# Optimization experiments

Hardware: AMD Instinct MI355X
Metric: run time of the kernel (lower is better)

Reference implementation:

```python
import jax, jax.numpy as jnp
import numpy as np

L, N, E = 2048, 2, 1024
H = 16                      # num_heads
DH = E // H                 # head_dim = 64
SCALE = DH ** -0.5
NEG = -10000.0


def setup_inputs() -> dict:
    key = jax.random.key(0)
    ks = jax.random.split(key, 9)
    s = 0.02
    return {
        "query": jax.random.normal(ks[0], (L, N, E), jnp.float32),
        "q_proj": jax.random.normal(ks[1], (E, E), jnp.float32) * s,
        "q_bias": jax.random.normal(ks[2], (E,), jnp.float32) * s,
        "k_proj": jax.random.normal(ks[3], (E, E), jnp.float32) * s,
        "k_bias": jax.random.normal(ks[4], (E,), jnp.float32) * s,
        "v_proj": jax.random.normal(ks[5], (E, E), jnp.float32) * s,
        "v_bias": jax.random.normal(ks[6], (E,), jnp.float32) * s,
        "out_proj": jax.random.normal(ks[7], (E, E), jnp.float32) * s,
        "out_bias": jax.random.normal(ks[8], (E,), jnp.float32) * s,
    }


def reference(query, q_proj, q_bias, k_proj, k_bias, v_proj, v_bias, out_proj, out_bias):
    # query: [L, N, E]; projections act as F.linear: x @ W.T + b
    q = query @ q_proj.T + q_bias
    k = query @ k_proj.T + k_bias
    v = query @ v_proj.T + v_bias
    # [L, N*H, DH] -> [N*H, L, DH]
    q = q.reshape(L, N * H, DH).transpose(1, 0, 2) * SCALE
    k = k.reshape(L, N * H, DH).transpose(1, 0, 2)
    v = v.reshape(L, N * H, DH).transpose(1, 0, 2)
    attn = jnp.einsum('bqd,bkd->bqk', q, k)  # [N*H, L, L]
    causal = jnp.tril(jnp.ones((L, L), jnp.float32)) < 0.5  # True above diagonal
    attn = jnp.where(causal[None, :, :], NEG, attn)
    attn = jax.nn.softmax(attn, axis=-1)
    # dropout_p = 0.0 in training mode -> identity
    out = jnp.einsum('bqk,bkd->bqd', attn, v)  # [N*H, L, DH]
    out = out.transpose(1, 0, 2).reshape(L, N, H * DH)
    return out @ out_proj.T + out_bias
```

## Files before the change

kernel.cpp:

```cpp
#include <hip/hip_runtime.h>
#include <stdint.h>

typedef __attribute__((ext_vector_type(8)))  short          bf16x8;
typedef __attribute__((ext_vector_type(4)))  float          f32x4;
typedef __attribute__((ext_vector_type(16))) float          f32x16;
typedef __attribute__((ext_vector_type(4)))  unsigned int   u32x4;
typedef __attribute__((ext_vector_type(4)))  unsigned short u16x4;

#define SCALE_LOG2E 0.180336880f

static __device__ __forceinline__ unsigned short f2bf(float x) {
  union { float f; unsigned int u; } c; c.f = x;
  unsigned int r = c.u + 0x7fffu + ((c.u >> 16) & 1u);
  return (unsigned short)(r >> 16);
}

static __device__ __forceinline__ unsigned int cvt_pk_bf16(float lo, float hi) {
  unsigned int r;
  asm volatile("v_cvt_pk_bf16_f32 %0, %1, %2" : "=v"(r) : "v"(lo), "v"(hi));
  return r;
}

static __device__ __forceinline__ void stage16(const unsigned short* g, unsigned short* l) {
  __builtin_amdgcn_global_load_lds(
      (const __attribute__((address_space(1))) unsigned int*)g,
      (__attribute__((address_space(3)))       unsigned int*)l, 16, 0, 0);
}

__global__ __launch_bounds__(256) void cvt_f32_bf16(const float* __restrict__ src,
                                                    unsigned short* __restrict__ dst, int n) {
  int i = (blockIdx.x * 256 + threadIdx.x) * 4;
  if (i < n) {
    float4 v = *(const float4*)(src + i);
    u16x4 o; o.x = f2bf(v.x); o.y = f2bf(v.y); o.z = f2bf(v.z); o.w = f2bf(v.w);
    *(u16x4*)(dst + i) = o;
  }
}

__global__ __launch_bounds__(256) void cvt_w4(const float* __restrict__ wq, const float* __restrict__ wk,
                                              const float* __restrict__ wv, const float* __restrict__ wo,
                                              unsigned short* __restrict__ dst) {
  const int z = blockIdx.y;
  const float* src = z == 0 ? wq : (z == 1 ? wk : (z == 2 ? wv : wo));
  int i = (blockIdx.x * 256 + threadIdx.x) * 4;
  float4 v = *(const float4*)(src + i);
  u16x4 o; o.x = f2bf(v.x); o.y = f2bf(v.y); o.z = f2bf(v.z); o.w = f2bf(v.w);
  *(u16x4*)(dst + (size_t)z * 1048576 + i) = o;
}

__device__ __forceinline__ void gemm_tile_core(const unsigned short* __restrict__ A,
                                               const unsigned short* __restrict__ B,
                                               int bi, int bj, f32x4 (&acc)[4][4]) {
  __shared__ unsigned short As[128 * 32];
  __shared__ unsigned short Bs[128 * 32];
  const int t = threadIdx.x, w = t >> 6, l = t & 63;
  const int l15 = l & 15, l4 = l >> 4;
  const int wm = w >> 1, wn = w & 1;
  const int srow = l >> 2, scol = (l & 3) * 8;

#pragma unroll
  for (int m = 0; m < 4; m++)
#pragma unroll
    for (int n = 0; n < 4; n++)
#pragma unroll
      for (int r = 0; r < 4; r++) acc[m][n][r] = 0.f;

  const int koff = 8 * l4;
  for (int k0 = 0; k0 < 1024; k0 += 32) {
    stage16(A + (size_t)(bi * 128 + w * 16 + srow) * 1024 + k0 + scol, (unsigned short*)As + w * 512);
    stage16(A + (size_t)(bi * 128 + (w + 4) * 16 + srow) * 1024 + k0 + scol, (unsigned short*)As + (w + 4) * 512);
    stage16(B + (size_t)(bj * 128 + w * 16 + srow) * 1024 + k0 + scol, (unsigned short*)Bs + w * 512);
    stage16(B + (size_t)(bj * 128 + (w + 4) * 16 + srow) * 1024 + k0 + scol, (unsigned short*)Bs + (w + 4) * 512);
    __syncthreads();

    bf16x8 af[4], bfr[4];
#pragma unroll
    for (int m = 0; m < 4; m++) af[m]  = *(const bf16x8*)(As + (wm * 64 + m * 16 + l15) * 32 + koff);
#pragma unroll
    for (int n = 0; n < 4; n++) bfr[n] = *(const bf16x8*)(Bs + (wn * 64 + n * 16 + l15) * 32 + koff);
#pragma unroll
    for (int m = 0; m < 4; m++)
#pragma unroll
      for (int n = 0; n < 4; n++)
        acc[m][n] = __builtin_amdgcn_mfma_f32_16x16x32_bf16(af[m], bfr[n], acc[m][n], 0, 0, 0);
    __syncthreads();
  }
}

__global__ __launch_bounds__(256) void gemm_qkv(
    const unsigned short* __restrict__ X,
    const unsigned short* __restrict__ Wq, const unsigned short* __restrict__ Wk,
    const unsigned short* __restrict__ Wv,
    const float* __restrict__ bq, const float* __restrict__ bk, const float* __restrict__ bv,
    unsigned short* __restrict__ Qf, unsigned short* __restrict__ Kf, unsigned short* __restrict__ Vf) {
  const int mode = blockIdx.z;
  const unsigned short* W = mode == 0 ? Wq : (mode == 1 ? Wk : Wv);
  const float* bias = mode == 0 ? bq : (mode == 1 ? bk : bv);
  f32x4 acc[4][4];
  gemm_tile_core(X, W, blockIdx.y, blockIdx.x, acc);

  const int t = threadIdx.x, w = t >> 6, l = t & 63;
  const int l15 = l & 15, l4 = l >> 4;
  const int wm = w >> 1, wn = w & 1;
  const int i0 = blockIdx.y * 128 + wm * 64 + 4 * l4;
  const int j0 = blockIdx.x * 128 + wn * 64 + l15;
#pragma unroll
  for (int m = 0; m < 4; m++)
#pragma unroll
    for (int n = 0; n < 4; n++) {
      const int j = j0 + n * 16;
      const float bv_ = bias[j];
      const int h = j >> 6, d = j & 63;
#pragma unroll
      for (int r = 0; r < 4; r++) {
        const int i = i0 + m * 16 + r;
        const int n_ = i & 1, ll = i >> 1;
        const int b = n_ * 16 + h;
        const int kt = ll >> 5, l31k = ll & 31;
        float v = acc[m][n][r] + bv_;
        if (mode == 0) {
          const int lane = l31k + 32 * ((d >> 3) & 1);
          Qf[((size_t)(b * 64 + kt) * 4 + (d >> 4)) * 512 + lane * 8 + (d & 7)] = f2bf(v * SCALE_LOG2E);
        } else if (mode == 1) {
          const int lane = l31k + 32 * ((d >> 3) & 1);
          Kf[((size_t)(b * 64 + kt) * 4 + (d >> 4)) * 512 + lane * 8 + (d & 7)] = f2bf(v);
        } else {
          const int j2 = 2 * (d >> 5) + ((l31k >> 4) & 1);
          const int lane = (d & 31) + 32 * ((l31k >> 3) & 1);
          Vf[((size_t)(b * 64 + kt) * 4 + j2) * 512 + lane * 8 + (l31k & 7)] = f2bf(v);
        }
      }
    }
}

__global__ __launch_bounds__(256) void gemm_out(
    const unsigned short* __restrict__ X2, const unsigned short* __restrict__ Wo,
    const float* __restrict__ bias, float* __restrict__ out) {
  f32x4 acc[4][4];
  gemm_tile_core(X2, Wo, blockIdx.y, blockIdx.x, acc);
  const int t = threadIdx.x, w = t >> 6, l = t & 63;
  const int l15 = l & 15, l4 = l >> 4;
  const int wm = w >> 1, wn = w & 1;
  const int i0 = blockIdx.y * 128 + wm * 64 + 4 * l4;
  const int j0 = blockIdx.x * 128 + wn * 64 + l15;
#pragma unroll
  for (int m = 0; m < 4; m++)
#pragma unroll
    for (int n = 0; n < 4; n++) {
      const int j = j0 + n * 16;
      const float bv_ = bias[j];
#pragma unroll
      for (int r = 0; r < 4; r++)
        out[(size_t)(i0 + m * 16 + r) * 1024 + j] = acc[m][n][r] + bv_;
    }
}

__global__ __launch_bounds__(256) void attn_kernel(
    const unsigned short* __restrict__ Qf, const unsigned short* __restrict__ Kf,
    const unsigned short* __restrict__ Vf, unsigned short* __restrict__ X2) {
  __shared__ float po[4 * 64 * 33];
  __shared__ float mbuf[4][32];
  __shared__ float lbuf[4][32];

  const unsigned id = blockIdx.x;
  const int rr = id >> 3;
  const int b = (id & 7) * 4 + (rr & 3);
  const int t = rr >> 2;

  const int w = threadIdx.x >> 6, l = threadIdx.x & 63;
  const int l31 = l & 31, g = l >> 5;

  const unsigned short* qp = Qf + ((size_t)(b * 64 + t) * 4) * 512 + l * 8;
  bf16x8 qf[4];
#pragma unroll
  for (int s = 0; s < 4; s++) qf[s] = *(const bf16x8*)(qp + s * 512);

  f32x16 o0, o1;
#pragma unroll
  for (int r = 0; r < 16; r++) { o0[r] = 0.f; o1[r] = 0.f; }
  float m_run = -1e30f, lsum = 0.f;

  const unsigned short* kb = Kf + (size_t)b * 131072;
  const unsigned short* vb = Vf + (size_t)b * 131072;

  int kt = w;
  bf16x8 kf[4], vf[4];
  if (kt <= t) {
    const unsigned short* kp = kb + kt * 2048 + l * 8;
    const unsigned short* vp = vb + kt * 2048 + l * 8;
#pragma unroll
    for (int s = 0; s < 4; s++) { kf[s] = *(const bf16x8*)(kp + s * 512); vf[s] = *(const bf16x8*)(vp + s * 512); }
  }

  for (; kt <= t; kt += 4) {
    bf16x8 kn[4], vn[4];
    const int ktn = kt + 4;
    if (ktn <= t) {
      const unsigned short* kp = kb + ktn * 2048 + l * 8;
      const unsigned short* vp = vb + ktn * 2048 + l * 8;
#pragma unroll
      for (int s = 0; s < 4; s++) { kn[s] = *(const bf16x8*)(kp + s * 512); vn[s] = *(const bf16x8*)(vp + s * 512); }
    }

    f32x16 sa;
#pragma unroll
    for (int r = 0; r < 16; r++) sa[r] = 0.f;
#pragma unroll
    for (int s = 0; s < 4; s++)
      sa = __builtin_amdgcn_mfma_f32_32x32x16_bf16(kf[s], qf[s], sa, 0, 0, 0);

    float p[16];
#pragma unroll
    for (int r = 0; r < 16; r++) p[r] = sa[r];
    if (kt == t) {
#pragma unroll
      for (int r = 0; r < 16; r++) {
        const int kvloc = (r & 3) + 8 * (r >> 2) + 4 * g;
        p[r] = (kvloc <= l31) ? p[r] : -30000.f;
      }
    }
    float mloc = p[0];
#pragma unroll
    for (int r = 1; r < 16; r++) mloc = fmaxf(mloc, p[r]);
    const float mtile = fmaxf(mloc, __shfl_xor(mloc, 32, 64));
    if (__any(mtile > m_run + 8.f)) {
      const float mnew = fmaxf(m_run, mtile);
      const float sc = exp2f(m_run - mnew);
      m_run = mnew;
      lsum *= sc;
#pragma unroll
      for (int r = 0; r < 16; r++) { o0[r] *= sc; o1[r] *= sc; }
    }
    float ps = 0.f;
#pragma unroll
    for (int r = 0; r < 16; r++) { p[r] = exp2f(p[r] - m_run); ps += p[r]; }
    lsum += ps;

    unsigned int u[8], pu[8];
#pragma unroll
    for (int i = 0; i < 8; i++) u[i] = cvt_pk_bf16(p[2 * i], p[2 * i + 1]);
#pragma unroll
    for (int i = 0; i < 8; i++) pu[i] = (unsigned int)__shfl_xor((int)u[i], 32, 64);
    u32x4 B0, B1;
    B0.x = g ? pu[2] : u[0];  B0.y = g ? pu[3] : u[1];
    B0.z = g ? u[2] : pu[0];  B0.w = g ? u[3] : pu[1];
    B1.x = g ? pu[6] : u[4];  B1.y = g ? pu[7] : u[5];
    B1.z = g ? u[6] : pu[4];  B1.w = g ? u[7] : pu[5];
    const bf16x8 pb0 = __builtin_bit_cast(bf16x8, B0);
    const bf16x8 pb1 = __builtin_bit_cast(bf16x8, B1);

    o0 = __builtin_amdgcn_mfma_f32_32x32x16_bf16(vf[0], pb0, o0, 0, 0, 0);
    o0 = __builtin_amdgcn_mfma_f32_32x32x16_bf16(vf[1], pb1, o0, 0, 0, 0);
    o1 = __builtin_amdgcn_mfma_f32_32x32x16_bf16(vf[2], pb0, o1, 0, 0, 0);
    o1 = __builtin_amdgcn_mfma_f32_32x32x16_bf16(vf[3], pb1, o1, 0, 0, 0);

#pragma unroll
    for (int s = 0; s < 4; s++) { kf[s] = kn[s]; vf[s] = vn[s]; }
  }

  const float lsum_full = lsum + __shfl_xor(lsum, 32, 64);
  float* mypo = po + (w * 64 + l) * 33;
#pragma unroll
  for (int r = 0; r < 16; r++) { mypo[r] = o0[r]; mypo[16 + r] = o1[r]; }
  if (l < 32) { mbuf[w][l] = m_run; lbuf[w][l] = lsum_full; }
  __syncthreads();

  float ms[4];
#pragma unroll
  for (int s = 0; s < 4; s++) ms[s] = mbuf[s][l31];
  const float mt = fmaxf(fmaxf(ms[0], ms[1]), fmaxf(ms[2], ms[3]));
  float scf[4]; float lt = 0.f;
#pragma unroll
  for (int s = 0; s < 4; s++) { scf[s] = exp2f(ms[s] - mt); lt += scf[s] * lbuf[s][l31]; }
  const float inv = 1.f / lt;

  float c0[4] = {0.f, 0.f, 0.f, 0.f}, c1[4] = {0.f, 0.f, 0.f, 0.f};
#pragma unroll
  for (int s = 0; s < 4; s++) {
    const float* pp = po + (s * 64 + l) * 33 + w * 4;
#pragma unroll
    for (int j = 0; j < 4; j++) { c0[j] += scf[s] * pp[j]; c1[j] += scf[s] * pp[16 + j]; }
  }

  const int n_ = b >> 4, h = b & 15;
  const int q0 = t * 32;
  unsigned short* orow = X2 + ((size_t)((q0 + l31) * 2 + n_)) * 1024 + h * 64;
#pragma unroll
  for (int j = 0; j < 4; j++) {
    const int d = j + 8 * w + 4 * g;
    orow[d]      = f2bf(c0[j] * inv);
    orow[32 + d] = f2bf(c1[j] * inv);
  }
}

extern "C" void kernel_launch(void* const* d_in, const int* in_sizes, int n_in,
                              void* d_out, int out_size, void* d_ws, size_t ws_size,
                              hipStream_t stream) {
  const float* query    = (const float*)d_in[0];
  const float* q_proj   = (const float*)d_in[1];
  const float* q_bias   = (const float*)d_in[2];
  const float* k_proj   = (const float*)d_in[3];
  const float* k_bias   = (const float*)d_in[4];
  const float* v_proj   = (const float*)d_in[5];
  const float* v_bias   = (const float*)d_in[6];
  const float* out_proj = (const float*)d_in[7];
  const float* out_bias = (const float*)d_in[8];
  float* out = (float*)d_out;

  char* ws = (char*)d_ws;
  unsigned short* Xq = (unsigned short*)(ws);
  unsigned short* Wq = (unsigned short*)(ws + (8u << 20));
  unsigned short* Qf = (unsigned short*)(ws + (16u << 20));
  unsigned short* Kf = (unsigned short*)(ws + (24u << 20));
  unsigned short* Vf = (unsigned short*)(ws + (32u << 20));
  unsigned short* X2 = (unsigned short*)(ws + (40u << 20));
  unsigned short* Wk = Wq + 1048576;
  unsigned short* Wv = Wq + 2097152;
  unsigned short* Wo = Wq + 3145728;

  cvt_f32_bf16<<<4096, 256, 0, stream>>>(query, Xq, 4194304);
  cvt_w4<<<dim3(1024, 4), 256, 0, stream>>>(q_proj, k_proj, v_proj, out_proj, Wq);

  gemm_qkv<<<dim3(8, 32, 3), 256, 0, stream>>>(Xq, Wq, Wk, Wv, q_bias, k_bias, v_bias, Qf, Kf, Vf);
  attn_kernel<<<2048, 256, 0, stream>>>(Qf, Kf, Vf, X2);
  gemm_out<<<dim3(8, 32), 256, 0, stream>>>(X2, Wo, out_bias, out);
}
```

Baseline: 127.5 us.

## Halve attention LDS scratch, reverse query-tile order, tree-reduce softmax max/sum

Shrinks the cross-wave output combine buffer from 33 to 17 floats per lane by writing and reducing o0 and o1 in two passes separated by extra barriers, which lowers LDS use per block and may allow more blocks per CU. Reverses the query-tile order so the longest causal tiles are scheduled first, to reduce tail imbalance. Replaces the serial max and sum chains with pairwise trees for more instruction-level parallelism, and drops volatile from the bf16 pack asm so the compiler can schedule it. The cost is two additional __syncthreads in the epilogue.

```diff
diff --git a/kernel.cpp b/kernel.cpp
--- a/kernel.cpp
+++ b/kernel.cpp
@@ -17,7 +17,7 @@
 
 static __device__ __forceinline__ unsigned int cvt_pk_bf16(float lo, float hi) {
   unsigned int r;
-  asm volatile("v_cvt_pk_bf16_f32 %0, %1, %2" : "=v"(r) : "v"(lo), "v"(hi));
+  asm("v_cvt_pk_bf16_f32 %0, %1, %2" : "=v"(r) : "v"(lo), "v"(hi));
   return r;
 }
 
@@ -158,14 +158,14 @@
 __global__ __launch_bounds__(256) void attn_kernel(
     const unsigned short* __restrict__ Qf, const unsigned short* __restrict__ Kf,
     const unsigned short* __restrict__ Vf, unsigned short* __restrict__ X2) {
-  __shared__ float po[4 * 64 * 33];
+  __shared__ float po[4 * 64 * 17];
   __shared__ float mbuf[4][32];
   __shared__ float lbuf[4][32];
 
   const unsigned id = blockIdx.x;
-  const int rr = id >> 3;
-  const int b = (id & 7) * 4 + (rr & 3);
-  const int t = rr >> 2;
+  const int s_ = id >> 3;
+  const int b = (id & 7) * 4 + (s_ & 3);
+  const int t = 63 - (s_ >> 2);
 
   const int w = threadIdx.x >> 6, l = threadIdx.x & 63;
   const int l31 = l & 31, g = l >> 5;
@@ -219,9 +219,10 @@
         p[r] = (kvloc <= l31) ? p[r] : -30000.f;
       }
     }
-    float mloc = p[0];
-#pragma unroll
-    for (int r = 1; r < 16; r++) mloc = fmaxf(mloc, p[r]);
+    float x0 = fmaxf(p[0], p[1]),  x1 = fmaxf(p[2], p[3]),  x2 = fmaxf(p[4], p[5]),  x3 = fmaxf(p[6], p[7]);
+    float x4 = fmaxf(p[8], p[9]),  x5 = fmaxf(p[10], p[11]), x6 = fmaxf(p[12], p[13]), x7 = fmaxf(p[14], p[15]);
+    x0 = fmaxf(x0, x1); x2 = fmaxf(x2, x3); x4 = fmaxf(x4, x5); x6 = fmaxf(x6, x7);
+    const float mloc = fmaxf(fmaxf(x0, x2), fmaxf(x4, x6));
     const float mtile = fmaxf(mloc, __shfl_xor(mloc, 32, 64));
     if (__any(mtile > m_run + 8.f)) {
       const float mnew = fmaxf(m_run, mtile);
@@ -231,10 +232,12 @@
 #pragma unroll
       for (int r = 0; r < 16; r++) { o0[r] *= sc; o1[r] *= sc; }
     }
-    float ps = 0.f;
-#pragma unroll
-    for (int r = 0; r < 16; r++) { p[r] = exp2f(p[r] - m_run); ps += p[r]; }
-    lsum += ps;
+#pragma unroll
+    for (int r = 0; r < 16; r++) p[r] = exp2f(p[r] - m_run);
+    float a0 = p[0] + p[1],  a1 = p[2] + p[3],  a2 = p[4] + p[5],  a3 = p[6] + p[7];
+    float a4 = p[8] + p[9],  a5 = p[10] + p[11], a6 = p[12] + p[13], a7 = p[14] + p[15];
+    a0 += a1; a2 += a3; a4 += a5; a6 += a7;
+    lsum += (a0 + a2) + (a4 + a6);
 
     unsigned int u[8], pu[8];
 #pragma unroll
@@ -259,9 +262,9 @@
   }
 
   const float lsum_full = lsum + __shfl_xor(lsum, 32, 64);
-  float* mypo = po + (w * 64 + l) * 33;
-#pragma unroll
-  for (int r = 0; r < 16; r++) { mypo[r] = o0[r]; mypo[16 + r] = o1[r]; }
+  float* mypo = po + (w * 64 + l) * 17;
+#pragma unroll
+  for (int r = 0; r < 16; r++) mypo[r] = o0[r];
   if (l < 32) { mbuf[w][l] = m_run; lbuf[w][l] = lsum_full; }
   __syncthreads();
 
@@ -277,9 +280,19 @@
   float c0[4] = {0.f, 0.f, 0.f, 0.f}, c1[4] = {0.f, 0.f, 0.f, 0.f};
 #pragma unroll
   for (int s = 0; s < 4; s++) {
-    const float* pp = po + (s * 64 + l) * 33 + w * 4;
-#pragma unroll
-    for (int j = 0; j < 4; j++) { c0[j] += scf[s] * pp[j]; c1[j] += scf[s] * pp[16 + j]; }
+    const float* pp = po + (s * 64 + l) * 17 + w * 4;
+#pragma unroll
+    for (int j = 0; j < 4; j++) c0[j] += scf[s] * pp[j];
+  }
+  __syncthreads();
+#pragma unroll
+  for (int r = 0; r < 16; r++) mypo[r] = o1[r];
+  __syncthreads();
+#pragma unroll
+  for (int s = 0; s < 4; s++) {
+    const float* pp = po + (s * 64 + l) * 17 + w * 4;
+#pragma unroll
+    for (int j = 0; j < 4; j++) c1[j] += scf[s] * pp[j];
   }
 
   const int n_ = b >> 4, h = b & 15;
```

Result: faster. 122.9 us (-3.6%).
